# Performance work log

Measured on AMD Instinct MI355X. Metric: run time of the kernel, lower is better.

The kernel has to match this reference:

```python
import jax, jax.numpy as jnp
import numpy as np

NUM_NODES = 1_000_000  # global node-state table size
N = 100_000            # batch of unique nodes
D = 128                # embedding dim
SIZE = 32              # map is SIZE x SIZE cells
C = SIZE * SIZE        # 1024 cells


def setup_inputs() -> dict:
    key = jax.random.key(0)
    k1, k2, k3, k4 = jax.random.split(key, 4)
    embeddings = jax.random.normal(k1, (N, D), dtype=jnp.float32)
    memory_map = jax.random.normal(k2, (C, D), dtype=jnp.float32)
    nodes = jax.random.randint(k3, (N,), 0, NUM_NODES, dtype=jnp.int64)
    times = jax.random.uniform(k4, (N,), dtype=jnp.float32)
    # node state tables: cell assignment initialized to -1 (unassigned), time to 0
    node_cell = jnp.full((NUM_NODES,), -1, dtype=jnp.int32)
    node_time = jnp.zeros((NUM_NODES,), dtype=jnp.float32)
    return {"embeddings": embeddings, "memory_map": memory_map,
            "nodes": nodes, "times": times,
            "node_cell": node_cell, "node_time": node_time}


def _euclidean_cdist(x, m):
    # torch.cdist(x, m, p=2): [N, C] pairwise L2 distances
    sq = (jnp.sum(x * x, axis=1, keepdims=True)
          + jnp.sum(m * m, axis=1)[None, :]
          - 2.0 * (x @ m.T))
    return jnp.sqrt(jnp.maximum(sq, 0.0))


def reference(embeddings, memory_map, nodes, times, node_cell, node_time):
    # find_center_distances: distance of each node embedding to every map cell,
    # nearest-cell assignment, then scatter update of the node state tables
    # (memory_map.set_nodes_distance(nodes, cells, times)).
    distances = _euclidean_cdist(embeddings, memory_map)      # [N, C]
    min_indices = jnp.argmin(distances, axis=1)               # [N]
    cells = min_indices.astype(jnp.int32)                     # list_num[min_indices] == min_indices
    new_node_cell = node_cell.at[nodes].set(cells)
    new_node_time = node_time.at[nodes].set(times)
    return distances, cells, new_node_cell, new_node_time
```

## Files before the change

kernel.cpp:

```cpp
#include <hip/hip_runtime.h>
#include <stdint.h>

constexpr int D_DIM   = 128;
constexpr int C_CELLS = 1024;
constexpr float EPS_D = 1.5e-3f;

typedef __attribute__((ext_vector_type(8))) short  short8;
typedef __attribute__((ext_vector_type(4))) float  floatx4;

#define GLOBAL_AS __attribute__((address_space(1)))
#define LDS_AS    __attribute__((address_space(3)))

__device__ __forceinline__ void gl2lds16(const void* g, void* l) {
    __builtin_amdgcn_global_load_lds((const GLOBAL_AS unsigned int*)g,
                                     (LDS_AS unsigned int*)l, 16, 0, 0);
}

__device__ __forceinline__ unsigned short f32_bf16_rtn(float x) {
    union { float f; unsigned u; } v; v.f = x;
    unsigned r = v.u + 0x7FFFu + ((v.u >> 16) & 1u);
    return (unsigned short)(r >> 16);
}
__device__ __forceinline__ float bf16_f32(unsigned short h) {
    union { float f; unsigned u; } v; v.u = ((unsigned)h) << 16; return v.f;
}
__device__ __forceinline__ float hi_f32(unsigned long long p) {
    union { float f; unsigned u; } v; v.u = (unsigned)(p >> 32); return v.f;
}

__global__ void init_kernel(int* win, int* flag, int* suspCount, int numNodes) {
    int j = blockIdx.x * blockDim.x + threadIdx.x;
    if (j < numNodes) win[j] = -1;
    if (j == 0) { *flag = 1; *suspCount = 0; }
}

__global__ void detect_kernel(const int* nodes32, int n, int* flag) {
    int i = blockIdx.x * blockDim.x + threadIdx.x;
    if (i < n && (i & 1) && nodes32[i] != 0) *flag = 0;
}

__global__ void winner_kernel(const void* nodes, int n, const int* flag, int* win) {
    int i = blockIdx.x * blockDim.x + threadIdx.x;
    if (i >= n) return;
    int node = (*flag) ? (int)((const long long*)nodes)[i]
                       : ((const int*)nodes)[i];
    atomicMax(&win[node], i);
}

__global__ void norms_kernel(const float* __restrict__ v, float* __restrict__ o, int rows) {
    int row  = blockIdx.x * 4 + (threadIdx.x >> 6);
    int lane = threadIdx.x & 63;
    if (row >= rows) return;
    float2 x = reinterpret_cast<const float2*>(v)[(size_t)row * 64 + lane];
    float s = x.x * x.x + x.y * x.y;
    #pragma unroll
    for (int m = 32; m; m >>= 1) s += __shfl_xor(s, m, 64);
    if (lane == 0) o[row] = s;
}

__global__ void convB_kernel(const float* __restrict__ M,
                             unsigned short* __restrict__ Bh_g,
                             unsigned short* __restrict__ Bl_g) {
    int idx  = blockIdx.x * 256 + threadIdx.x;
    int cell = idx >> 4;
    int b    = idx & 15;
    const float4* s = reinterpret_cast<const float4*>(M + (size_t)cell * D_DIM + b * 8);
    float4 v0 = s[0], v1 = s[1];
    float xv[8] = { v0.x, v0.y, v0.z, v0.w, v1.x, v1.y, v1.z, v1.w };
    short8 hs, ls;
    #pragma unroll
    for (int j = 0; j < 8; ++j) {
        unsigned short hb = f32_bf16_rtn(xv[j]);
        unsigned short lb = f32_bf16_rtn(xv[j] - bf16_f32(hb));
        hs[j] = (short)hb; ls[j] = (short)lb;
    }
    int tile = cell >> 6, r = cell & 63;
    int dst = tile * 8192 + r * 128 + ((b ^ (r & 15)) << 3);
    *reinterpret_cast<short8*>(&Bh_g[dst]) = hs;
    *reinterpret_cast<short8*>(&Bl_g[dst]) = ls;
}

__global__ __launch_bounds__(256, 3)
void dist_kernel(const float* __restrict__ X,
                 const unsigned short* __restrict__ Bh_g,
                 const unsigned short* __restrict__ Bl_g,
                 const float* __restrict__ msq,
                 float* __restrict__ outD, int* __restrict__ cells32,
                 int* __restrict__ suspects, int* __restrict__ suspCount,
                 int N)
{
    __shared__ __align__(16) unsigned short ldsH[64 * 128];
    __shared__ __align__(16) unsigned short ldsL[64 * 128];
    __shared__ float msq_s[C_CELLS];
    __shared__ float Axs[64];
    __shared__ unsigned long long sp1[64][2];
    __shared__ float              sm2[64][2];

    const int tid  = threadIdx.x;
    const int lane = tid & 63;
    const int wave = tid >> 6;
    const int q    = lane >> 4;
    const int l15  = lane & 15;
    const int w0   = wave & 1;
    const int w1   = wave >> 1;
    const int blockRow = blockIdx.x * 64;
    const bool fullBlock = (blockRow + 64 <= N);

    #pragma unroll
    for (int p = 0; p < 4; ++p) {
        int r = p * 16 + (tid >> 4);
        int b = tid & 15;
        int gRow = blockRow + r;
        float4 v0 = make_float4(0.f, 0.f, 0.f, 0.f), v1 = v0;
        if (gRow < N) {
            const float4* s = reinterpret_cast<const float4*>(X + (size_t)gRow * D_DIM + b * 8);
            v0 = s[0]; v1 = s[1];
        }
        float xv[8] = { v0.x, v0.y, v0.z, v0.w, v1.x, v1.y, v1.z, v1.w };
        short8 hs, ls;
        float sq = 0.f;
        #pragma unroll
        for (int j = 0; j < 8; ++j) {
            sq += xv[j] * xv[j];
            unsigned short hb = f32_bf16_rtn(xv[j]);
            unsigned short lb = f32_bf16_rtn(xv[j] - bf16_f32(hb));
            hs[j] = (short)hb; ls[j] = (short)lb;
        }
        #pragma unroll
        for (int m = 1; m < 16; m <<= 1) sq += __shfl_xor(sq, m, 16);
        if (b == 0) Axs[r] = sq;
        int ad = r * 128 + ((b ^ (r & 15)) << 3);
        *reinterpret_cast<short8*>(&ldsH[ad]) = hs;
        *reinterpret_cast<short8*>(&ldsL[ad]) = ls;
    }
    {
        float4 mv = *reinterpret_cast<const float4*>(&msq[tid * 4]);
        *reinterpret_cast<float4*>(&msq_s[tid * 4]) = mv;
    }
    __syncthreads();

    short8 xh[2][4], xl[2][4];
    #pragma unroll
    for (int t = 0; t < 2; ++t)
        #pragma unroll
        for (int kc = 0; kc < 4; ++kc) {
            int row = w1 * 32 + t * 16 + l15;
            int ad  = row * 128 + (((kc * 4 + q) ^ l15) << 3);
            xh[t][kc] = *reinterpret_cast<const short8*>(&ldsH[ad]);
            xl[t][kc] = *reinterpret_cast<const short8*>(&ldsL[ad]);
        }
    float xs[2];
    xs[0] = Axs[w1 * 32 + l15];
    xs[1] = Axs[w1 * 32 + 16 + l15];
    __syncthreads();

    {
        const char* bhg = (const char*)Bh_g + wave * 4096 + lane * 16;
        const char* blg = (const char*)Bl_g + wave * 4096 + lane * 16;
        char* bhl = (char*)ldsH + wave * 4096;
        char* bll = (char*)ldsL + wave * 4096;
        #pragma unroll
        for (int j = 0; j < 4; ++j) {
            gl2lds16(bhg + j * 1024, bhl + j * 1024);
            gl2lds16(blg + j * 1024, bll + j * 1024);
        }
    }
    asm volatile("s_waitcnt vmcnt(0)" ::: "memory");
    __builtin_amdgcn_sched_barrier(0);
    __builtin_amdgcn_s_barrier();
    __builtin_amdgcn_sched_barrier(0);

    float m1[2]  = { INFINITY, INFINITY };
    float m2v[2] = { INFINITY, INFINITY };
    int   c1[2]  = { 0, 0 };

    for (int ct = 0; ct < 16; ++ct) {
        floatx4 acc[2][2];
        #pragma unroll
        for (int t = 0; t < 2; ++t)
            #pragma unroll
            for (int u = 0; u < 2; ++u)
                acc[t][u] = (floatx4){0.f, 0.f, 0.f, 0.f};

        #pragma unroll
        for (int kc = 0; kc < 4; ++kc) {
            short8 mh[2], ml[2];
            #pragma unroll
            for (int u = 0; u < 2; ++u) {
                int cell = w0 * 32 + u * 16 + l15;
                int ad   = cell * 128 + (((kc * 4 + q) ^ l15) << 3);
                mh[u] = *reinterpret_cast<const short8*>(&ldsH[ad]);
                ml[u] = *reinterpret_cast<const short8*>(&ldsL[ad]);
            }
            #pragma unroll
            for (int t = 0; t < 2; ++t)
                #pragma unroll
                for (int u = 0; u < 2; ++u) {
                    acc[t][u] = __builtin_amdgcn_mfma_f32_16x16x32_bf16(mh[u], xh[t][kc], acc[t][u], 0, 0, 0);
                    acc[t][u] = __builtin_amdgcn_mfma_f32_16x16x32_bf16(mh[u], xl[t][kc], acc[t][u], 0, 0, 0);
                    acc[t][u] = __builtin_amdgcn_mfma_f32_16x16x32_bf16(ml[u], xh[t][kc], acc[t][u], 0, 0, 0);
                }
        }

        floatx4 dv[2][2];
        #pragma unroll
        for (int u = 0; u < 2; ++u) {
            int cbase = ct * 64 + w0 * 32 + u * 16 + q * 4;
            float4 ms4 = *reinterpret_cast<const float4*>(&msq_s[cbase]);
            float msv[4] = { ms4.x, ms4.y, ms4.z, ms4.w };
            #pragma unroll
            for (int t = 0; t < 2; ++t) {
                #pragma unroll
                for (int r = 0; r < 4; ++r) {
                    float s = fmaf(-2.0f, acc[t][u][r], xs[t] + msv[r]);
                    dv[t][u][r] = __builtin_amdgcn_sqrtf(fmaxf(s, 0.0f));
                    m2v[t] = __builtin_amdgcn_fmed3f(s, m1[t], m2v[t]);
                    c1[t]  = (s < m1[t]) ? (cbase + r) : c1[t];
                    m1[t]  = fminf(s, m1[t]);
                }
            }
        }

        __builtin_amdgcn_s_barrier();
        __builtin_amdgcn_sched_barrier(0);
        if (ct < 15) {
            const char* bhg = (const char*)Bh_g + (size_t)(ct + 1) * 16384 + wave * 4096 + lane * 16;
            const char* blg = (const char*)Bl_g + (size_t)(ct + 1) * 16384 + wave * 4096 + lane * 16;
            char* bhl = (char*)ldsH + wave * 4096;
            char* bll = (char*)ldsL + wave * 4096;
            #pragma unroll
            for (int j = 0; j < 4; ++j) {
                gl2lds16(bhg + j * 1024, bhl + j * 1024);
                gl2lds16(blg + j * 1024, bll + j * 1024);
            }
        }
        #pragma unroll
        for (int t = 0; t < 2; ++t) {
            int grow = blockRow + w1 * 32 + t * 16 + l15;
            if (grow < N) {
                size_t rb = (size_t)grow * C_CELLS + ct * 64 + w0 * 32 + q * 4;
                __builtin_nontemporal_store(dv[t][0], reinterpret_cast<floatx4*>(&outD[rb]));
                __builtin_nontemporal_store(dv[t][1], reinterpret_cast<floatx4*>(&outD[rb + 16]));
            }
        }
        __builtin_amdgcn_sched_barrier(0);
        if (ct < 15) {
            if (fullBlock) asm volatile("s_waitcnt vmcnt(4)" ::: "memory");
            else           asm volatile("s_waitcnt vmcnt(0)" ::: "memory");
            __builtin_amdgcn_sched_barrier(0);
            __builtin_amdgcn_s_barrier();
            __builtin_amdgcn_sched_barrier(0);
        }
    }

    #pragma unroll
    for (int t = 0; t < 2; ++t) {
        float a1 = m1[t], a2 = m2v[t]; int ac = c1[t];
        #pragma unroll
        for (int off = 16; off <= 32; off <<= 1) {
            float b1 = __shfl_xor(a1, off, 64);
            float b2 = __shfl_xor(a2, off, 64);
            int   bc = __shfl_xor(ac, off, 64);
            float hi = fmaxf(a1, b1);
            ac = (b1 < a1) ? bc : ac;
            a1 = fminf(a1, b1);
            a2 = fminf(fminf(a2, b2), hi);
        }
        if (q == 0) {
            int lr = w1 * 32 + t * 16 + l15;
            float d1 = __builtin_amdgcn_sqrtf(fmaxf(a1, 0.0f));
            float d2 = __builtin_amdgcn_sqrtf(fmaxf(a2, 0.0f));
            union { float f; unsigned u; } bu; bu.f = d1;
            sp1[lr][w0] = ((unsigned long long)bu.u << 32) | (unsigned)ac;
            sm2[lr][w0] = d2;
        }
    }
    __syncthreads();
    if (tid < 64) {
        int g = blockRow + tid;
        if (g < N) {
            unsigned long long a = sp1[tid][0], b = sp1[tid][1];
            unsigned long long G1 = (a < b) ? a : b;
            unsigned long long hi = (a < b) ? b : a;
            float M2  = fminf(fminf(sm2[tid][0], sm2[tid][1]), hi_f32(hi));
            float g1v = hi_f32(G1);
            cells32[g] = (int)(G1 & 0xffffffffu);
            if (M2 - g1v < EPS_D) {
                int ix = atomicAdd(suspCount, 1);
                suspects[ix] = g;
            }
        }
    }
}

__global__ __launch_bounds__(256)
void refine_kernel(const float* __restrict__ X, const float* __restrict__ M,
                   const int* __restrict__ suspects, const int* __restrict__ suspCount,
                   int* __restrict__ cells32)
{
    __shared__ double xd[128];
    __shared__ unsigned long long wres[4];
    int cnt = *suspCount;
    for (int s = blockIdx.x; s < cnt; s += gridDim.x) {
        int row = suspects[s];
        if (threadIdx.x < 128) xd[threadIdx.x] = (double)X[(size_t)row * D_DIM + threadIdx.x];
        __syncthreads();
        unsigned long long best = ~0ull;
        for (int c = threadIdx.x; c < C_CELLS; c += 256) {
            const float* mp = M + (size_t)c * D_DIM;
            double acc = 0.0;
            #pragma unroll 4
            for (int k = 0; k < D_DIM; ++k) {
                double diff = xd[k] - (double)mp[k];
                acc = fma(diff, diff, acc);
            }
            unsigned long long bits = (unsigned long long)__double_as_longlong(acc);
            unsigned long long pk = (bits & ~1023ull) | (unsigned long long)c;
            if (pk < best) best = pk;
        }
        #pragma unroll
        for (int m = 32; m; m >>= 1) {
            unsigned long long o = __shfl_xor(best, m, 64);
            if (o < best) best = o;
        }
        if ((threadIdx.x & 63) == 0) wres[threadIdx.x >> 6] = best;
        __syncthreads();
        if (threadIdx.x == 0) {
            unsigned long long b0 = wres[0] < wres[1] ? wres[0] : wres[1];
            unsigned long long b1 = wres[2] < wres[3] ? wres[2] : wres[3];
            unsigned long long b  = b0 < b1 ? b0 : b1;
            cells32[row] = (int)(b & 1023ull);
        }
        __syncthreads();
    }
}

__global__ void post_kernel(const int* __restrict__ cells32,
                            const int* __restrict__ win,
                            const float* __restrict__ times,
                            const int* __restrict__ node_cell,
                            const float* __restrict__ node_time,
                            float* __restrict__ outCells,
                            float* __restrict__ outNC,
                            float* __restrict__ outNT,
                            int n, int numNodes)
{
    int j = blockIdx.x * blockDim.x + threadIdx.x;
    if (j < n) outCells[j] = (float)cells32[j];
    if (j < numNodes) {
        int w = win[j];
        float c, t;
        if (w >= 0) {
            c = (float)cells32[w];
            t = times[w];
        } else {
            c = (float)node_cell[j];
            t = node_time[j];
        }
        outNC[j] = c;
        outNT[j] = t;
    }
}

extern "C" void kernel_launch(void* const* d_in, const int* in_sizes, int n_in,
                              void* d_out, int out_size, void* d_ws, size_t ws_size,
                              hipStream_t stream)
{
    const float* X         = (const float*)d_in[0];
    const float* M         = (const float*)d_in[1];
    const void*  nodes     = d_in[2];
    const float* times     = (const float*)d_in[3];
    const int*   node_cell = (const int*)d_in[4];
    const float* node_time = (const float*)d_in[5];

    const int N        = in_sizes[3];
    const int numNodes = in_sizes[4];
    const int C        = in_sizes[1] / D_DIM;

    char* ws = (char*)d_ws;
    size_t off = 0;
    unsigned short* Bh_g = (unsigned short*)(ws + off); off += (size_t)C * D_DIM * 2;
    unsigned short* Bl_g = (unsigned short*)(ws + off); off += (size_t)C * D_DIM * 2;
    int* win      = (int*)(ws + off); off += (size_t)numNodes * 4;
    int* cells32  = (int*)(ws + off); off += (size_t)N * 4;
    int* suspects = (int*)(ws + off); off += (size_t)N * 4;
    float* msq    = (float*)(ws + off); off += (size_t)C * 4;
    int* flag     = (int*)(ws + off); off += 4;
    int* suspCount= (int*)(ws + off); off += 4;
    (void)ws_size; (void)n_in; (void)out_size;

    float* outD     = (float*)d_out;
    float* outCells = outD + (size_t)N * C;
    float* outNC    = outCells + N;
    float* outNT    = outNC + numNodes;

    init_kernel  <<<(numNodes + 255) / 256, 256, 0, stream>>>(win, flag, suspCount, numNodes);
    detect_kernel<<<(N + 255) / 256, 256, 0, stream>>>((const int*)nodes, N, flag);
    winner_kernel<<<(N + 255) / 256, 256, 0, stream>>>(nodes, N, flag, win);
    norms_kernel <<<(C + 3) / 4, 256, 0, stream>>>(M, msq, C);
    convB_kernel <<<(C * 16 + 255) / 256, 256, 0, stream>>>(M, Bh_g, Bl_g);
    dist_kernel  <<<(N + 63) / 64, 256, 0, stream>>>(X, Bh_g, Bl_g, msq, outD, cells32,
                                                     suspects, suspCount, N);
    refine_kernel<<<512, 256, 0, stream>>>(X, M, suspects, suspCount, cells32);
    post_kernel  <<<(numNodes + 255) / 256, 256, 0, stream>>>(cells32, win, times, node_cell,
                                                              node_time, outCells, outNC, outNT,
                                                              N, numNodes);
}
```

Before: 589.5 us.

## Stage distance tiles through LDS for full-row coalesced stores; fuse norms into convB

The distance tile is now written to a swizzled LDS staging buffer, then read back so each wave stores contiguous 256-byte row segments of the output matrix, replacing scattered 16-byte stores. The stage area aliases the Axs region, and sp1/sm2 alias msq_s, in one manually laid-out shared buffer. The cell squared-norm computation moves into the bf16 conversion kernel via a 16-lane shuffle reduction, removing one launch. The change adds an LDS round trip and an lgkmcnt wait before the barrier in each tile iteration, and the larger shared footprint may reduce occupancy.

```diff
diff --git a/kernel.cpp b/kernel.cpp
--- a/kernel.cpp
+++ b/kernel.cpp
@@ -47,20 +47,10 @@
     atomicMax(&win[node], i);
 }
 
-__global__ void norms_kernel(const float* __restrict__ v, float* __restrict__ o, int rows) {
-    int row  = blockIdx.x * 4 + (threadIdx.x >> 6);
-    int lane = threadIdx.x & 63;
-    if (row >= rows) return;
-    float2 x = reinterpret_cast<const float2*>(v)[(size_t)row * 64 + lane];
-    float s = x.x * x.x + x.y * x.y;
-    #pragma unroll
-    for (int m = 32; m; m >>= 1) s += __shfl_xor(s, m, 64);
-    if (lane == 0) o[row] = s;
-}
-
 __global__ void convB_kernel(const float* __restrict__ M,
                              unsigned short* __restrict__ Bh_g,
-                             unsigned short* __restrict__ Bl_g) {
+                             unsigned short* __restrict__ Bl_g,
+                             float* __restrict__ msq) {
     int idx  = blockIdx.x * 256 + threadIdx.x;
     int cell = idx >> 4;
     int b    = idx & 15;
@@ -68,12 +58,17 @@
     float4 v0 = s[0], v1 = s[1];
     float xv[8] = { v0.x, v0.y, v0.z, v0.w, v1.x, v1.y, v1.z, v1.w };
     short8 hs, ls;
+    float sq = 0.f;
     #pragma unroll
     for (int j = 0; j < 8; ++j) {
+        sq += xv[j] * xv[j];
         unsigned short hb = f32_bf16_rtn(xv[j]);
         unsigned short lb = f32_bf16_rtn(xv[j] - bf16_f32(hb));
         hs[j] = (short)hb; ls[j] = (short)lb;
     }
+    #pragma unroll
+    for (int m = 1; m < 16; m <<= 1) sq += __shfl_xor(sq, m, 16);
+    if (b == 0) msq[cell] = sq;
     int tile = cell >> 6, r = cell & 63;
     int dst = tile * 8192 + r * 128 + ((b ^ (r & 15)) << 3);
     *reinterpret_cast<short8*>(&Bh_g[dst]) = hs;
@@ -89,12 +84,14 @@
                  int* __restrict__ suspects, int* __restrict__ suspCount,
                  int N)
 {
-    __shared__ __align__(16) unsigned short ldsH[64 * 128];
-    __shared__ __align__(16) unsigned short ldsL[64 * 128];
-    __shared__ float msq_s[C_CELLS];
-    __shared__ float Axs[64];
-    __shared__ unsigned long long sp1[64][2];
-    __shared__ float              sm2[64][2];
+    __shared__ __align__(16) char smem[53248];
+    unsigned short* ldsH  = reinterpret_cast<unsigned short*>(smem);
+    unsigned short* ldsL  = reinterpret_cast<unsigned short*>(smem + 16384);
+    float*          stage = reinterpret_cast<float*>(smem + 32768);
+    float*          msq_s = reinterpret_cast<float*>(smem + 49152);
+    float*          Axs   = reinterpret_cast<float*>(smem + 32768);
+    unsigned long long* sp1 = reinterpret_cast<unsigned long long*>(smem + 49152);
+    float*          sm2   = reinterpret_cast<float*>(smem + 49152 + 1024);
 
     const int tid  = threadIdx.x;
     const int lane = tid & 63;
@@ -202,7 +199,6 @@
                 }
         }
 
-        floatx4 dv[2][2];
         #pragma unroll
         for (int u = 0; u < 2; ++u) {
             int cbase = ct * 64 + w0 * 32 + u * 16 + q * 4;
@@ -210,17 +206,24 @@
             float msv[4] = { ms4.x, ms4.y, ms4.z, ms4.w };
             #pragma unroll
             for (int t = 0; t < 2; ++t) {
+                floatx4 dvv;
                 #pragma unroll
                 for (int r = 0; r < 4; ++r) {
                     float s = fmaf(-2.0f, acc[t][u][r], xs[t] + msv[r]);
-                    dv[t][u][r] = __builtin_amdgcn_sqrtf(fmaxf(s, 0.0f));
+                    dvv[r] = __builtin_amdgcn_sqrtf(fmaxf(s, 0.0f));
                     m2v[t] = __builtin_amdgcn_fmed3f(s, m1[t], m2v[t]);
                     c1[t]  = (s < m1[t]) ? (cbase + r) : c1[t];
                     m1[t]  = fminf(s, m1[t]);
                 }
-            }
-        }
-
+                int row  = w1 * 32 + t * 16 + l15;
+                int u4   = w0 * 8 + u * 4 + q;
+                int unit = row * 16 + (u4 ^ l15);
+                *reinterpret_cast<floatx4*>(&stage[unit * 4]) = dvv;
+            }
+        }
+
+        asm volatile("s_waitcnt lgkmcnt(0)" ::: "memory");
+        __builtin_amdgcn_sched_barrier(0);
         __builtin_amdgcn_s_barrier();
         __builtin_amdgcn_sched_barrier(0);
         if (ct < 15) {
@@ -235,12 +238,14 @@
             }
         }
         #pragma unroll
-        for (int t = 0; t < 2; ++t) {
-            int grow = blockRow + w1 * 32 + t * 16 + l15;
+        for (int j = 0; j < 4; ++j) {
+            int row = (wave << 4) + ((j >> 1) << 3) + (lane >> 3);
+            int u4r = (lane & 7) + ((j & 1) << 3);
+            floatx4 v = *reinterpret_cast<const floatx4*>(&stage[(row * 16 + (u4r ^ (row & 15))) * 4]);
+            int grow = blockRow + row;
             if (grow < N) {
-                size_t rb = (size_t)grow * C_CELLS + ct * 64 + w0 * 32 + q * 4;
-                __builtin_nontemporal_store(dv[t][0], reinterpret_cast<floatx4*>(&outD[rb]));
-                __builtin_nontemporal_store(dv[t][1], reinterpret_cast<floatx4*>(&outD[rb + 16]));
+                __builtin_nontemporal_store(v,
+                    reinterpret_cast<floatx4*>(&outD[(size_t)grow * C_CELLS + ct * 64 + u4r * 4]));
             }
         }
         __builtin_amdgcn_sched_barrier(0);
@@ -271,18 +276,18 @@
             float d1 = __builtin_amdgcn_sqrtf(fmaxf(a1, 0.0f));
             float d2 = __builtin_amdgcn_sqrtf(fmaxf(a2, 0.0f));
             union { float f; unsigned u; } bu; bu.f = d1;
-            sp1[lr][w0] = ((unsigned long long)bu.u << 32) | (unsigned)ac;
-            sm2[lr][w0] = d2;
+            sp1[lr * 2 + w0] = ((unsigned long long)bu.u << 32) | (unsigned)ac;
+            sm2[lr * 2 + w0] = d2;
         }
     }
     __syncthreads();
     if (tid < 64) {
         int g = blockRow + tid;
         if (g < N) {
-            unsigned long long a = sp1[tid][0], b = sp1[tid][1];
+            unsigned long long a = sp1[tid * 2 + 0], b = sp1[tid * 2 + 1];
             unsigned long long G1 = (a < b) ? a : b;
             unsigned long long hi = (a < b) ? b : a;
-            float M2  = fminf(fminf(sm2[tid][0], sm2[tid][1]), hi_f32(hi));
+            float M2  = fminf(fminf(sm2[tid * 2 + 0], sm2[tid * 2 + 1]), hi_f32(hi));
             float g1v = hi_f32(G1);
             cells32[g] = (int)(G1 & 0xffffffffu);
             if (M2 - g1v < EPS_D) {
@@ -397,8 +402,7 @@
     init_kernel  <<<(numNodes + 255) / 256, 256, 0, stream>>>(win, flag, suspCount, numNodes);
     detect_kernel<<<(N + 255) / 256, 256, 0, stream>>>((const int*)nodes, N, flag);
     winner_kernel<<<(N + 255) / 256, 256, 0, stream>>>(nodes, N, flag, win);
-    norms_kernel <<<(C + 3) / 4, 256, 0, stream>>>(M, msq, C);
-    convB_kernel <<<(C * 16 + 255) / 256, 256, 0, stream>>>(M, Bh_g, Bl_g);
+    convB_kernel <<<(C * 16 + 255) / 256, 256, 0, stream>>>(M, Bh_g, Bl_g, msq);
     dist_kernel  <<<(N + 63) / 64, 256, 0, stream>>>(X, Bh_g, Bl_g, msq, outD, cells32,
                                                      suspects, suspCount, N);
     refine_kernel<<<512, 256, 0, stream>>>(X, M, suspects, suspCount, cells32);
```

Result: faster. 577.4 us (-2.1%).
